# Kernel optimization log

Hardware: AMD Instinct MI355X
Metric: run time of the kernel (lower is better)

Reference implementation:

```python
import jax, jax.numpy as jnp
from jax import lax
import numpy as np

B, C, H, W = 4, 512, 128, 128
K = 19  # n_cls / object regions


def setup_inputs() -> dict:
    key = jax.random.key(0)
    k1, k2, k3 = jax.random.split(key, 3)
    context = jax.random.normal(k1, (B, K, H, W), dtype=jnp.float32)
    feature = jax.random.normal(k2, (B, C, H, W), dtype=jnp.float32)
    w1 = jnp.zeros((C, C, 1, 1), dtype=jnp.float32)  # zero-init per _zero_init_conv
    b1 = jnp.zeros((C,), dtype=jnp.float32)
    w2 = jax.random.normal(k3, (K, 2 * C, 3, 3), dtype=jnp.float32) * 0.02
    b2 = jnp.zeros((K,), dtype=jnp.float32)
    return {"context": context, "feature": feature, "w1": w1, "b1": b1, "w2": w2, "b2": b2}


def reference(context, feature, w1, b1, w2, b2):
    b, c, h, w = feature.shape
    hw = h * w
    f = feature.reshape(b, c, hw).transpose(0, 2, 1)          # [B, HW, C]
    ctx = context.reshape(b, context.shape[1], hw)            # [B, K, HW]
    attn = jax.nn.softmax(ctx, axis=2)                        # softmax over HW
    ocr = jnp.einsum('bkn,bnc->bck', attn, f)                 # ocr_context [B, C, K]
    rel = jnp.einsum('bnc,bck->bkn', f, ocr)                  # relation (already transposed) [B, K, HW]
    attn2 = jax.nn.softmax(rel, axis=2)                       # softmax over HW
    res = jnp.einsum('bck,bkn->bcn', ocr, attn2).reshape(b, c, h, w)
    dn = ('NCHW', 'OIHW', 'NCHW')
    res = lax.conv_general_dilated(res, w1, (1, 1), 'VALID', dimension_numbers=dn)
    res = res + b1[None, :, None, None]
    cat = jnp.concatenate([res, feature], axis=1)             # [B, 2C, H, W]
    out = lax.conv_general_dilated(cat, w2, (1, 1), ((1, 1), (1, 1)), dimension_numbers=dn)
    out = out + b2[None, :, None, None]
    return out
```

## Files before the change

### kernel.cpp

```cpp
#include <hip/hip_runtime.h>
#include <math.h>


#define BB 4
#define KK 19
#define CC 512
#define HH 128
#define WW 128
#define HWHW (HH*WW)

__global__ __launch_bounds__(256) void softmax_rows(const float* __restrict__ in,
                                                    float* __restrict__ out) {
    int row = blockIdx.x;
    const float* r = in + (size_t)row * HWHW;
    float* o = out + (size_t)row * HWHW;
    int t = threadIdx.x;
    float v[64];
    float m = -1e30f;
#pragma unroll
    for (int i = 0; i < 64; ++i) { v[i] = r[t + i * 256]; m = fmaxf(m, v[i]); }
    for (int off = 32; off; off >>= 1) m = fmaxf(m, __shfl_xor(m, off));
    __shared__ float sm[4], ss[4];
    int wave = t >> 6;
    if ((t & 63) == 0) sm[wave] = m;
    __syncthreads();
    m = fmaxf(fmaxf(sm[0], sm[1]), fmaxf(sm[2], sm[3]));
    float s = 0.f;
#pragma unroll
    for (int i = 0; i < 64; ++i) { v[i] = __expf(v[i] - m); s += v[i]; }
    for (int off = 32; off; off >>= 1) s += __shfl_xor(s, off);
    if ((t & 63) == 0) ss[wave] = s;
    __syncthreads();
    s = ss[0] + ss[1] + ss[2] + ss[3];
    float inv = 1.f / s;
#pragma unroll
    for (int i = 0; i < 64; ++i) o[t + i * 256] = v[i] * inv;
}

#define NSPLIT 8
__global__ __launch_bounds__(256) void ocr_kernel(const float* __restrict__ feature,
                                                  const float* __restrict__ attn,
                                                  float* __restrict__ ocr) {
    int ctile = blockIdx.x, b = blockIdx.y, ns = blockIdx.z;
    int t = threadIdx.x, wave = t >> 6, lane = t & 63;
    int c0 = ctile * 16 + wave * 4;
    const float* fbase = feature + (size_t)b * CC * HWHW;
    const float* abase = attn + (size_t)b * KK * HWHW;
    float acc[4][KK];
#pragma unroll
    for (int j = 0; j < 4; ++j)
#pragma unroll
        for (int k = 0; k < KK; ++k) acc[j][k] = 0.f;
    int nstart = ns * (HWHW / NSPLIT);
    for (int it = 0; it < (HWHW / NSPLIT) / 64; ++it) {
        int n = nstart + it * 64 + lane;
        float a[KK];
#pragma unroll
        for (int k = 0; k < KK; ++k) a[k] = abase[(size_t)k * HWHW + n];
#pragma unroll
        for (int j = 0; j < 4; ++j) {
            float f = fbase[(size_t)(c0 + j) * HWHW + n];
#pragma unroll
            for (int k = 0; k < KK; ++k) acc[j][k] += f * a[k];
        }
    }
#pragma unroll
    for (int j = 0; j < 4; ++j)
#pragma unroll
        for (int k = 0; k < KK; ++k) {
            float x = acc[j][k];
            for (int off = 32; off; off >>= 1) x += __shfl_xor(x, off);
            if (lane == 0) atomicAdd(&ocr[((size_t)b * CC + (c0 + j)) * KK + k], x);
        }
}

__global__ __launch_bounds__(64) void ocr2_kernel(const float* __restrict__ w1,
                                                  const float* __restrict__ ocr,
                                                  float* __restrict__ ocr2) {
    int co = blockIdx.x, b = blockIdx.y, lane = threadIdx.x;
    float acc[KK];
#pragma unroll
    for (int k = 0; k < KK; ++k) acc[k] = 0.f;
    const float* wrow = w1 + (size_t)co * CC;
    const float* ob = ocr + (size_t)b * CC * KK;
    for (int ci = lane; ci < CC; ci += 64) {
        float w = wrow[ci];
#pragma unroll
        for (int k = 0; k < KK; ++k) acc[k] += w * ob[ci * KK + k];
    }
#pragma unroll
    for (int k = 0; k < KK; ++k) {
        float x = acc[k];
        for (int off = 32; off; off >>= 1) x += __shfl_xor(x, off);
        if (lane == 0) ocr2[((size_t)b * CC + co) * KK + k] = x;
    }
}

__global__ __launch_bounds__(256) void wtr_kernel(const float* __restrict__ w2,
                                                  float* __restrict__ wTr) {
    int idx = blockIdx.x * 256 + threadIdx.x;
    if (idx >= CC * 171) return;
    int c = idx / 171, j = idx % 171;
    int ko = j / 9, dydx = j % 9;
    wTr[idx] = w2[((size_t)ko * (2 * CC) + CC + c) * 9 + dydx];
}

__global__ __launch_bounds__(64) void w2a_kernel(const float* __restrict__ w2,
                                                 const float* __restrict__ ocr2,
                                                 const float* __restrict__ b1,
                                                 float* __restrict__ w2a,
                                                 float* __restrict__ bcon) {
    int ko = blockIdx.x, dydx = blockIdx.y, b = blockIdx.z, lane = threadIdx.x;
    float acc[KK];
#pragma unroll
    for (int k = 0; k < KK; ++k) acc[k] = 0.f;
    float accb = 0.f;
    for (int c = lane; c < CC; c += 64) {
        float wv = w2[((size_t)ko * (2 * CC) + c) * 9 + dydx];
#pragma unroll
        for (int k = 0; k < KK; ++k) acc[k] += wv * ocr2[((size_t)b * CC + c) * KK + k];
        accb += wv * b1[c];
    }
#pragma unroll
    for (int k = 0; k < KK; ++k) {
        float x = acc[k];
        for (int off = 32; off; off >>= 1) x += __shfl_xor(x, off);
        if (lane == 0) w2a[(((size_t)b * KK + ko) * KK + k) * 9 + dydx] = x;
    }
    for (int off = 32; off; off >>= 1) accb += __shfl_xor(accb, off);
    if (lane == 0 && b == 0) bcon[ko * 9 + dydx] = accb;
}

#define NSREL 4
__global__ __launch_bounds__(256) void rel_kernel(const float* __restrict__ feature,
                                                  const float* __restrict__ ocr,
                                                  float* __restrict__ rel) {
    int b = blockIdx.y, ns = blockIdx.z;
    int n = blockIdx.x * 256 + threadIdx.x;
    int cbase = ns * (CC / NSREL);
    const float* fb = feature + ((size_t)b * CC + cbase) * HWHW + n;
    const float* ob = ocr + ((size_t)b * CC + cbase) * KK;
    float acc[KK];
#pragma unroll
    for (int k = 0; k < KK; ++k) acc[k] = 0.f;
    for (int ci = 0; ci < CC / NSREL; ++ci) {
        float f = fb[(size_t)ci * HWHW];
#pragma unroll
        for (int k = 0; k < KK; ++k) acc[k] += ob[ci * KK + k] * f;
    }
#pragma unroll
    for (int k = 0; k < KK; ++k)
        atomicAdd(&rel[((size_t)b * KK + k) * HWHW + n], acc[k]);
}

#define NSOUT 8
__global__ __launch_bounds__(256) void out_kernel(const float* __restrict__ feature,
                                                  const float* __restrict__ attn2,
                                                  const float* __restrict__ wTr,
                                                  const float* __restrict__ w2a,
                                                  const float* __restrict__ bcon,
                                                  const float* __restrict__ b2,
                                                  float* __restrict__ out) {
    int b = blockIdx.y, ns = blockIdx.z;
    int t = threadIdx.x;
    int y = blockIdx.x * 2 + (t >> 7);
    int x = t & 127;

    float m[9];
    int off[9];
#pragma unroll
    for (int dy = -1; dy <= 1; ++dy)
#pragma unroll
        for (int dx = -1; dx <= 1; ++dx) {
            int i = (dy + 1) * 3 + (dx + 1);
            int yy = y + dy, xx = x + dx;
            bool valid = (yy >= 0 && yy < HH && xx >= 0 && xx < WW);
            m[i] = valid ? 1.f : 0.f;
            int yc = min(max(yy, 0), HH - 1), xc = min(max(xx, 0), WW - 1);
            off[i] = yc * WW + xc;
        }

    float acc[KK];
#pragma unroll
    for (int ko = 0; ko < KK; ++ko) acc[ko] = 0.f;

    if (ns == 0) {
#pragma unroll
        for (int ko = 0; ko < KK; ++ko) acc[ko] = b2[ko];
#pragma unroll
        for (int i = 0; i < 9; ++i)
#pragma unroll
            for (int ko = 0; ko < KK; ++ko) acc[ko] += m[i] * bcon[ko * 9 + i];
        const float* a2b = attn2 + (size_t)b * KK * HWHW;
        const float* wab = w2a + (size_t)b * KK * KK * 9;
        for (int k = 0; k < KK; ++k) {
            float tap[9];
#pragma unroll
            for (int i = 0; i < 9; ++i) tap[i] = m[i] * a2b[(size_t)k * HWHW + off[i]];
#pragma unroll
            for (int ko = 0; ko < KK; ++ko)
#pragma unroll
                for (int i = 0; i < 9; ++i) acc[ko] += wab[(ko * KK + k) * 9 + i] * tap[i];
        }
    }

    int cbase = ns * (CC / NSOUT);
    const float* fb = feature + ((size_t)b * CC + cbase) * HWHW;
    for (int cc = 0; cc < CC / NSOUT; ++cc) {
        float tap[9];
#pragma unroll
        for (int i = 0; i < 9; ++i) tap[i] = m[i] * fb[(size_t)cc * HWHW + off[i]];
        const float* wr = wTr + (cbase + cc) * 171;
#pragma unroll
        for (int j = 0; j < 171; ++j) acc[j / 9] += wr[j] * tap[j % 9];
    }

    size_t obase = ((size_t)b * KK) * HWHW + (size_t)y * WW + x;
#pragma unroll
    for (int ko = 0; ko < KK; ++ko) atomicAdd(&out[obase + (size_t)ko * HWHW], acc[ko]);
}

extern "C" void kernel_launch(void* const* d_in, const int* in_sizes, int n_in,
                              void* d_out, int out_size, void* d_ws, size_t ws_size,
                              hipStream_t stream) {
    const float* ctx = (const float*)d_in[0];
    const float* feature = (const float*)d_in[1];
    const float* w1 = (const float*)d_in[2];
    const float* b1 = (const float*)d_in[3];
    const float* w2 = (const float*)d_in[4];
    const float* b2 = (const float*)d_in[5];
    float* out = (float*)d_out;

    float* ws = (float*)d_ws;
    float* attn = ws;
    float* ocr = attn + (size_t)BB * KK * HWHW;
    float* ocr2 = ocr + (size_t)BB * CC * KK;
    float* w2a = ocr2 + (size_t)BB * CC * KK;
    float* bcon = w2a + (size_t)BB * KK * KK * 9;
    float* wTr = bcon + KK * 9;

    hipMemsetAsync(ocr, 0, (size_t)BB * CC * KK * sizeof(float), stream);
    hipMemsetAsync(out, 0, (size_t)out_size * sizeof(float), stream);

    softmax_rows<<<BB * KK, 256, 0, stream>>>(ctx, attn);
    ocr_kernel<<<dim3(CC / 16, BB, NSPLIT), 256, 0, stream>>>(feature, attn, ocr);
    ocr2_kernel<<<dim3(CC, BB), 64, 0, stream>>>(w1, ocr, ocr2);
    wtr_kernel<<<(CC * 171 + 255) / 256, 256, 0, stream>>>(w2, wTr);
    w2a_kernel<<<dim3(KK, 9, BB), 64, 0, stream>>>(w2, ocr2, b1, w2a, bcon);
    hipMemsetAsync(attn, 0, (size_t)BB * KK * HWHW * sizeof(float), stream);
    rel_kernel<<<dim3(HWHW / 256, BB, NSREL), 256, 0, stream>>>(feature, ocr, attn);
    softmax_rows<<<BB * KK, 256, 0, stream>>>(attn, attn);
    out_kernel<<<dim3(HH / 2, BB, NSOUT), 256, 0, stream>>>(feature, attn, wTr, w2a, bcon, b2, out);
}
```

Baseline: 551.1 us.

## Pack feature, ocr and conv weights to fp16 pairs and use fdot2

The ocr kernel now also writes an fp16 channel-pair packed copy of the feature map. The rel and out kernels read this packed copy, along with packed ocr and packed w2 weights, and accumulate with v_dot2 fp16 instructions into fp32. This halves the feature bytes read by the two heavy passes and halves their multiply instruction count. In exchange it adds an fp16 write pass and loses precision in the relation logits, which then feed a softmax. NSPLIT is also raised to 16.

```diff
diff --git a/kernel.cpp b/kernel.cpp
--- a/kernel.cpp
+++ b/kernel.cpp
@@ -1,10 +1,13 @@
 #include <hip/hip_runtime.h>
 #include <math.h>
 
+
+typedef _Float16 h2 __attribute__((ext_vector_type(2)));
 
 #define BB 4
 #define KK 19
 #define CC 512
+#define C2 (CC/2)
 #define HH 128
 #define WW 128
 #define HWHW (HH*WW)
@@ -37,15 +40,17 @@
     for (int i = 0; i < 64; ++i) o[t + i * 256] = v[i] * inv;
 }
 
-#define NSPLIT 8
+#define NSPLIT 16
 __global__ __launch_bounds__(256) void ocr_kernel(const float* __restrict__ feature,
                                                   const float* __restrict__ attn,
-                                                  float* __restrict__ ocr) {
+                                                  float* __restrict__ ocr,
+                                                  h2* __restrict__ fpk) {
     int ctile = blockIdx.x, b = blockIdx.y, ns = blockIdx.z;
     int t = threadIdx.x, wave = t >> 6, lane = t & 63;
     int c0 = ctile * 16 + wave * 4;
     const float* fbase = feature + (size_t)b * CC * HWHW;
     const float* abase = attn + (size_t)b * KK * HWHW;
+    h2* fpb = fpk + (size_t)b * C2 * HWHW;
     float acc[4][KK];
 #pragma unroll
     for (int j = 0; j < 4; ++j)
@@ -57,12 +62,18 @@
         float a[KK];
 #pragma unroll
         for (int k = 0; k < KK; ++k) a[k] = abase[(size_t)k * HWHW + n];
-#pragma unroll
-        for (int j = 0; j < 4; ++j) {
-            float f = fbase[(size_t)(c0 + j) * HWHW + n];
-#pragma unroll
-            for (int k = 0; k < KK; ++k) acc[j][k] += f * a[k];
-        }
+        float fv[4];
+#pragma unroll
+        for (int j = 0; j < 4; ++j) fv[j] = fbase[(size_t)(c0 + j) * HWHW + n];
+        h2 p0, p1;
+        p0[0] = (_Float16)fv[0]; p0[1] = (_Float16)fv[1];
+        p1[0] = (_Float16)fv[2]; p1[1] = (_Float16)fv[3];
+        fpb[(size_t)(c0 >> 1) * HWHW + n] = p0;
+        fpb[(size_t)((c0 >> 1) + 1) * HWHW + n] = p1;
+#pragma unroll
+        for (int j = 0; j < 4; ++j)
+#pragma unroll
+            for (int k = 0; k < KK; ++k) acc[j][k] += fv[j] * a[k];
     }
 #pragma unroll
     for (int j = 0; j < 4; ++j)
@@ -96,13 +107,29 @@
     }
 }
 
-__global__ __launch_bounds__(256) void wtr_kernel(const float* __restrict__ w2,
-                                                  float* __restrict__ wTr) {
+__global__ __launch_bounds__(256) void wpk_kernel(const float* __restrict__ w2,
+                                                  h2* __restrict__ wpk) {
     int idx = blockIdx.x * 256 + threadIdx.x;
-    if (idx >= CC * 171) return;
-    int c = idx / 171, j = idx % 171;
-    int ko = j / 9, dydx = j % 9;
-    wTr[idx] = w2[((size_t)ko * (2 * CC) + CC + c) * 9 + dydx];
+    if (idx >= C2 * 171) return;
+    int c2 = idx / 171, j = idx % 171;
+    int ko = j / 9, tap = j % 9;
+    h2 p;
+    p[0] = (_Float16)w2[((size_t)ko * (2 * CC) + CC + 2 * c2) * 9 + tap];
+    p[1] = (_Float16)w2[((size_t)ko * (2 * CC) + CC + 2 * c2 + 1) * 9 + tap];
+    wpk[idx] = p;
+}
+
+__global__ __launch_bounds__(256) void opk_kernel(const float* __restrict__ ocr,
+                                                  h2* __restrict__ opk) {
+    int b = blockIdx.x, c2 = threadIdx.x;
+    const float* ob = ocr + (size_t)b * CC * KK;
+    h2* op = opk + (size_t)b * C2 * KK;
+    for (int k = 0; k < KK; ++k) {
+        h2 p;
+        p[0] = (_Float16)ob[(2 * c2) * KK + k];
+        p[1] = (_Float16)ob[(2 * c2 + 1) * KK + k];
+        op[c2 * KK + k] = p;
+    }
 }
 
 __global__ __launch_bounds__(64) void w2a_kernel(const float* __restrict__ w2,
@@ -132,21 +159,22 @@
 }
 
 #define NSREL 4
-__global__ __launch_bounds__(256) void rel_kernel(const float* __restrict__ feature,
-                                                  const float* __restrict__ ocr,
+__global__ __launch_bounds__(256) void rel_kernel(const h2* __restrict__ fpk,
+                                                  const h2* __restrict__ opk,
                                                   float* __restrict__ rel) {
     int b = blockIdx.y, ns = blockIdx.z;
     int n = blockIdx.x * 256 + threadIdx.x;
-    int cbase = ns * (CC / NSREL);
-    const float* fb = feature + ((size_t)b * CC + cbase) * HWHW + n;
-    const float* ob = ocr + ((size_t)b * CC + cbase) * KK;
+    int cb = ns * (C2 / NSREL);
+    const h2* fb = fpk + ((size_t)b * C2 + cb) * HWHW + n;
+    const h2* ob = opk + ((size_t)b * C2 + cb) * KK;
     float acc[KK];
 #pragma unroll
     for (int k = 0; k < KK; ++k) acc[k] = 0.f;
-    for (int ci = 0; ci < CC / NSREL; ++ci) {
-        float f = fb[(size_t)ci * HWHW];
-#pragma unroll
-        for (int k = 0; k < KK; ++k) acc[k] += ob[ci * KK + k] * f;
+    for (int c2 = 0; c2 < C2 / NSREL; ++c2) {
+        h2 f = fb[(size_t)c2 * HWHW];
+#pragma unroll
+        for (int k = 0; k < KK; ++k)
+            acc[k] = __builtin_amdgcn_fdot2(f, ob[c2 * KK + k], acc[k], false);
     }
 #pragma unroll
     for (int k = 0; k < KK; ++k)
@@ -154,9 +182,9 @@
 }
 
 #define NSOUT 8
-__global__ __launch_bounds__(256) void out_kernel(const float* __restrict__ feature,
+__global__ __launch_bounds__(256) void out_kernel(const h2* __restrict__ fpk,
                                                   const float* __restrict__ attn2,
-                                                  const float* __restrict__ wTr,
+                                                  const h2* __restrict__ wpk,
                                                   const float* __restrict__ w2a,
                                                   const float* __restrict__ bcon,
                                                   const float* __restrict__ b2,
@@ -204,15 +232,18 @@
         }
     }
 
-    int cbase = ns * (CC / NSOUT);
-    const float* fb = feature + ((size_t)b * CC + cbase) * HWHW;
-    for (int cc = 0; cc < CC / NSOUT; ++cc) {
-        float tap[9];
-#pragma unroll
-        for (int i = 0; i < 9; ++i) tap[i] = m[i] * fb[(size_t)cc * HWHW + off[i]];
-        const float* wr = wTr + (cbase + cc) * 171;
-#pragma unroll
-        for (int j = 0; j < 171; ++j) acc[j / 9] += wr[j] * tap[j % 9];
+    h2 hz; hz[0] = (_Float16)0.f; hz[1] = (_Float16)0.f;
+    int cb = ns * (C2 / NSOUT);
+    const h2* fb = fpk + ((size_t)b * C2 + cb) * HWHW;
+    for (int c2 = 0; c2 < C2 / NSOUT; ++c2) {
+        h2 tap2[9];
+#pragma unroll
+        for (int i = 0; i < 9; ++i)
+            tap2[i] = (m[i] != 0.f) ? fb[(size_t)c2 * HWHW + off[i]] : hz;
+        const h2* wr = wpk + (cb + c2) * 171;
+#pragma unroll
+        for (int j = 0; j < 171; ++j)
+            acc[j / 9] = __builtin_amdgcn_fdot2(wr[j], tap2[j % 9], acc[j / 9], false);
     }
 
     size_t obase = ((size_t)b * KK) * HWHW + (size_t)y * WW + x;
@@ -237,18 +268,21 @@
     float* ocr2 = ocr + (size_t)BB * CC * KK;
     float* w2a = ocr2 + (size_t)BB * CC * KK;
     float* bcon = w2a + (size_t)BB * KK * KK * 9;
-    float* wTr = bcon + KK * 9;
+    h2* fpk = (h2*)(bcon + KK * 9 + 1);
+    h2* opk = fpk + (size_t)BB * C2 * HWHW;
+    h2* wpk = opk + (size_t)BB * C2 * KK;
 
     hipMemsetAsync(ocr, 0, (size_t)BB * CC * KK * sizeof(float), stream);
     hipMemsetAsync(out, 0, (size_t)out_size * sizeof(float), stream);
 
     softmax_rows<<<BB * KK, 256, 0, stream>>>(ctx, attn);
-    ocr_kernel<<<dim3(CC / 16, BB, NSPLIT), 256, 0, stream>>>(feature, attn, ocr);
+    ocr_kernel<<<dim3(CC / 16, BB, NSPLIT), 256, 0, stream>>>(feature, attn, ocr, fpk);
     ocr2_kernel<<<dim3(CC, BB), 64, 0, stream>>>(w1, ocr, ocr2);
-    wtr_kernel<<<(CC * 171 + 255) / 256, 256, 0, stream>>>(w2, wTr);
+    wpk_kernel<<<(C2 * 171 + 255) / 256, 256, 0, stream>>>(w2, wpk);
     w2a_kernel<<<dim3(KK, 9, BB), 64, 0, stream>>>(w2, ocr2, b1, w2a, bcon);
+    opk_kernel<<<BB, 256, 0, stream>>>(ocr, opk);
     hipMemsetAsync(attn, 0, (size_t)BB * KK * HWHW * sizeof(float), stream);
-    rel_kernel<<<dim3(HWHW / 256, BB, NSREL), 256, 0, stream>>>(feature, ocr, attn);
+    rel_kernel<<<dim3(HWHW / 256, BB, NSREL), 256, 0, stream>>>(fpk, opk, attn);
     softmax_rows<<<BB * KK, 256, 0, stream>>>(attn, attn);
-    out_kernel<<<dim3(HH / 2, BB, NSOUT), 256, 0, stream>>>(feature, attn, wTr, w2a, bcon, b2, out);
-}
+    out_kernel<<<dim3(HH / 2, BB, NSOUT), 256, 0, stream>>>(fpk, attn, wpk, w2a, bcon, b2, out);
+}
```

Result: slower. 574.0 us (+4.1%).
